# Kernel tuning notes

Measured on AMD Instinct MI355X. Metric: run time of the kernel, lower is better.

Reference implementation:

```python
import jax, jax.numpy as jnp
import numpy as np

NUM_HEADS = 16
SLICE_SIZE = 1024
SCALING = SLICE_SIZE ** 0.5  # module divides by sqrt(slice_size), as written


def setup_inputs() -> dict:
    key = jax.random.key(0)
    ks = jax.random.split(key, 9)
    B, S, D = 4, 2048, SLICE_SIZE
    sc = 0.02
    return {
        "x": jax.random.normal(ks[0], (B, S, D), dtype=jnp.float32),
        "Wq": jax.random.normal(ks[1], (D, D), dtype=jnp.float32) * sc,
        "bq": jax.random.normal(ks[2], (D,), dtype=jnp.float32) * sc,
        "Wk": jax.random.normal(ks[3], (D, D), dtype=jnp.float32) * sc,
        "bk": jax.random.normal(ks[4], (D,), dtype=jnp.float32) * sc,
        "Wv": jax.random.normal(ks[5], (D, D), dtype=jnp.float32) * sc,
        "bv": jax.random.normal(ks[6], (D,), dtype=jnp.float32) * sc,
        "Wp": jax.random.normal(ks[7], (D, D), dtype=jnp.float32) * sc,
        "bp": jax.random.normal(ks[8], (D,), dtype=jnp.float32) * sc,
    }


def _split_heads(t):
    # 'b s (h o) -> b h s o'
    b, s, d = t.shape
    return t.reshape(b, s, NUM_HEADS, d // NUM_HEADS).transpose(0, 2, 1, 3)


def reference(x, Wq, bq, Wk, bk, Wv, bv, Wp, bp):
    q = _split_heads(x @ Wq.T + bq)  # [B,H,S,O]
    k = _split_heads(x @ Wk.T + bk)
    v = _split_heads(x @ Wv.T + bv)
    energy = jnp.einsum('bhqo,bhko->bhqk', q, k)  # full score matrix
    attn = jax.nn.softmax(energy / SCALING, axis=-1)
    # Faithful to source: 'b h q k, b h v o -> b h v o' sums attn over (q,k)
    out = jnp.einsum('bhqk,bhvo->bhvo', attn, v)
    b, h, s, o = out.shape
    out = out.transpose(0, 2, 1, 3).reshape(b, s, h * o)  # 'b h v o -> b v (h o)'
    return out @ Wp.T + bp
```

## Files before the change

kernel.cpp:

```cpp
#include <hip/hip_runtime.h>
#include <cstdint>


typedef unsigned short u16;
typedef __bf16 bf16x8 __attribute__((ext_vector_type(8)));
typedef float f32x4 __attribute__((ext_vector_type(4)));

__device__ __forceinline__ u16 f2bf(float f) {
  unsigned int u = __float_as_uint(f);
  u += 0x7fffu + ((u >> 16) & 1u);
  return (u16)(u >> 16);
}

__device__ __forceinline__ void load16(const void* g, void* l) {
  auto gp = (const __attribute__((address_space(1))) unsigned int*)(uintptr_t)g;
  auto lp = (__attribute__((address_space(3))) unsigned int*)(unsigned int)(uintptr_t)l;
  __builtin_amdgcn_global_load_lds(gp, lp, 16, 0, 0);
}

__global__ void k_prep(const float* __restrict__ x, const float* __restrict__ Wv,
                       const float* __restrict__ bv, const float* __restrict__ Wp,
                       const float* __restrict__ bp, u16* __restrict__ xb,
                       u16* __restrict__ wpb, u16* __restrict__ wvtb,
                       float* __restrict__ cv) {
  __shared__ float tile[32][33];
  const int b = blockIdx.x;
  const int tid = threadIdx.x;
  if (b < 9216) {
    const float* src = (b < 8192) ? x : Wp;
    u16* dst = (b < 8192) ? xb : wpb;
    const long base = (long)((b < 8192) ? b : (b - 8192)) * 1024 + tid * 4;
    const float4 v = *(const float4*)(src + base);
    ushort4 o;
    o.x = f2bf(v.x); o.y = f2bf(v.y); o.z = f2bf(v.z); o.w = f2bf(v.w);
    *(ushort4*)(dst + base) = o;
  } else if (b < 10240) {
    const int tb = b - 9216;
    const int bi = (tb & 31) * 32;
    const int bj = (tb >> 5) * 32;
    const int tx = tid & 31;
    const int ty = tid >> 5;
    for (int r = ty; r < 32; r += 8)
      tile[r][tx] = Wv[(long)(bj + r) * 1024 + bi + tx];
    __syncthreads();
    for (int r = ty; r < 32; r += 8)
      wvtb[(long)(bi + r) * 1024 + bj + tx] = f2bf(tile[tx][r]);
  } else {
    const int row = (b - 10240) * 4 + (tid >> 6);
    const int lane = tid & 63;
    const float* w = Wp + (long)row * 1024;
    float s = 0.f;
    for (int j = lane; j < 1024; j += 64) s += w[j] * bv[j];
    for (int off = 32; off; off >>= 1) s += __shfl_down(s, off, 64);
    if (lane == 0) cv[row] = 2048.f * s + bp[row];
  }
}

template <int MODE>
__global__ __launch_bounds__(256) void k_gemm(
    const u16* __restrict__ A, const u16* __restrict__ B, void* __restrict__ OutV,
    const float* __restrict__ bias, int M, int N, int K) {
  __shared__ u16 As[2][128 * 64];
  __shared__ u16 Bs[2][128 * 64];

  const int tid = threadIdx.x;
  const int lane = tid & 63;
  const int wv = tid >> 6;
  const int waveM = (wv & 1) << 6;
  const int waveN = (wv >> 1) << 6;
  const int l15 = lane & 15;
  const int quad = lane >> 4;

  long bm, bn;
  if constexpr (MODE == 0) {
    const int id = blockIdx.x;
    const int xcd = id & 7;
    const int j = id >> 3;
    const int nb = N >> 7;
    const int mPerXcd = M / 128 / 8;
    bm = (long)(xcd * mPerXcd + j / nb) * 128;
    bn = (long)(j % nb) * 128;
  } else {
    bm = (long)(blockIdx.x >> 3) * 128;
    bn = (long)(blockIdx.x & 7) * 128;
  }

  const int rsl = lane >> 3;
  const int cs = (lane & 7) ^ rsl;
  const u16* Ag0 = A + (bm + wv * 8 + rsl) * (long)K + cs * 8;
  const u16* Bg0 = B + (bn + wv * 8 + rsl) * (long)K + cs * 8;

  const int nT = K >> 6;

  auto STAGE = [&](long k0, int b) {
    u16* Ad = &As[b][0] + (wv << 9);
    u16* Bd = &Bs[b][0] + (wv << 9);
#pragma unroll
    for (int r = 0; r < 4; ++r) {
      load16(Ag0 + k0 + (long)(r * 32) * K, Ad + (r << 11));
      load16(Bg0 + k0 + (long)(r * 32) * K, Bd + (r << 11));
    }
  };

  const f32x4 zero = {0.f, 0.f, 0.f, 0.f};
  f32x4 acc[4][4];
#pragma unroll
  for (int i = 0; i < 4; ++i)
#pragma unroll
    for (int j = 0; j < 4; ++j) acc[i][j] = zero;

  const int rq0 = quad ^ (l15 & 7);
  const int rq1 = (4 + quad) ^ (l15 & 7);

  STAGE(0, 0);
  asm volatile("s_waitcnt vmcnt(0)" ::: "memory");
  __builtin_amdgcn_s_barrier();

  int cur = 0;
  for (int t = 0; t < nT; ++t) {
    const bool more = (t + 1) < nT;
    if (more) STAGE((long)(t + 1) << 6, cur ^ 1);
    __builtin_amdgcn_sched_barrier(0);

    const u16* Asb = &As[cur][0];
    const u16* Bsb = &Bs[cur][0];
    bf16x8 af[2][4], bg[2][4];
#pragma unroll
    for (int tt = 0; tt < 4; ++tt) {
      const int ra = (waveM + tt * 16 + l15) * 64;
      const int rb = (waveN + tt * 16 + l15) * 64;
      af[0][tt] = *(const bf16x8*)(Asb + ra + rq0 * 8);
      af[1][tt] = *(const bf16x8*)(Asb + ra + rq1 * 8);
      bg[0][tt] = *(const bf16x8*)(Bsb + rb + rq0 * 8);
      bg[1][tt] = *(const bf16x8*)(Bsb + rb + rq1 * 8);
    }
    asm volatile("s_waitcnt lgkmcnt(0)" ::: "memory");
    __builtin_amdgcn_sched_barrier(0);

#pragma unroll
    for (int kk = 0; kk < 2; ++kk)
#pragma unroll
      for (int i = 0; i < 4; ++i)
#pragma unroll
        for (int j = 0; j < 4; ++j)
          acc[i][j] = __builtin_amdgcn_mfma_f32_16x16x32_bf16(af[kk][i], bg[kk][j],
                                                              acc[i][j], 0, 0, 0);

    if (more) {
      asm volatile("s_waitcnt vmcnt(0)" ::: "memory");
      __builtin_amdgcn_s_barrier();
      cur ^= 1;
    }
  }

#pragma unroll
  for (int i = 0; i < 4; ++i) {
    const long gm = bm + waveM + i * 16 + quad * 4;
#pragma unroll
    for (int j = 0; j < 4; ++j) {
      const long gn = bn + waveN + j * 16 + l15;
      if constexpr (MODE == 0) {
        float* outp = (float*)OutV;
        const float bb = bias[gn];
#pragma unroll
        for (int r = 0; r < 4; ++r)
          outp[(gm + r) * N + gn] = acc[i][j][r] + bb;
      } else {
        u16* outp = (u16*)OutV;
#pragma unroll
        for (int r = 0; r < 4; ++r)
          outp[(gm + r) * N + gn] = f2bf(acc[i][j][r] * 2048.f);
      }
    }
  }
}

extern "C" void kernel_launch(void* const* d_in, const int* in_sizes, int n_in,
                              void* d_out, int out_size, void* d_ws, size_t ws_size,
                              hipStream_t stream) {
  const float* x  = (const float*)d_in[0];
  const float* Wv = (const float*)d_in[5];
  const float* bv = (const float*)d_in[6];
  const float* Wp = (const float*)d_in[7];
  const float* bp = (const float*)d_in[8];

  char* ws = (char*)d_ws;
  u16* xb    = (u16*)(ws);
  u16* wpb   = (u16*)(ws + (16u << 20));
  u16* wvtb  = (u16*)(ws + (18u << 20));
  u16* m2b   = (u16*)(ws + (20u << 20));
  float* cv  = (float*)(ws + (22u << 20));

  k_prep<<<10496, 256, 0, stream>>>(x, Wv, bv, Wp, bp, xb, wpb, wvtb, cv);

  k_gemm<1><<<64, 256, 0, stream>>>(wpb, wvtb, m2b, nullptr, 1024, 1024, 1024);

  k_gemm<0><<<512, 256, 0, stream>>>(xb, m2b, d_out, cv, 8192, 1024, 1024);
}
```

Baseline: 140.5 us.

## Deepen GEMM pipeline to four-stage LDS ring with K=32 tiles

Changes the GEMM mainloop from a double-buffered K=64 tile to a four-buffer ring of K=32 tiles with three tiles prefetched in flight. Partial vmcnt waits let global loads overlap more iterations of MFMA work, aimed at hiding memory latency in the load-bound GEMMs. The swizzle pattern is reworked for the narrower rows. Each iteration now has half the MFMA work per barrier, which doubles the number of barriers and may reduce LDS read efficiency.

New measurement: 144.8 us. +3.0%, slower.

```diff
diff --git a/kernel.cpp b/kernel.cpp
--- a/kernel.cpp
+++ b/kernel.cpp
@@ -60,8 +60,8 @@
 __global__ __launch_bounds__(256) void k_gemm(
     const u16* __restrict__ A, const u16* __restrict__ B, void* __restrict__ OutV,
     const float* __restrict__ bias, int M, int N, int K) {
-  __shared__ u16 As[2][128 * 64];
-  __shared__ u16 Bs[2][128 * 64];
+  __shared__ u16 As[4][128 * 32];
+  __shared__ u16 Bs[4][128 * 32];
 
   const int tid = threadIdx.x;
   const int lane = tid & 63;
@@ -85,21 +85,22 @@
     bn = (long)(blockIdx.x & 7) * 128;
   }
 
-  const int rsl = lane >> 3;
-  const int cs = (lane & 7) ^ rsl;
-  const u16* Ag0 = A + (bm + wv * 8 + rsl) * (long)K + cs * 8;
-  const u16* Bg0 = B + (bn + wv * 8 + rsl) * (long)K + cs * 8;
+  const int rl = lane >> 2;
+  const int cs = (lane & 3) ^ ((lane >> 3) & 3);
+  const u16* Ag0 = A + (bm + wv * 16 + rl) * (long)K + cs * 8;
+  const u16* Bg0 = B + (bn + wv * 16 + rl) * (long)K + cs * 8;
+  const long rowOff = 64 * (long)K;
 
-  const int nT = K >> 6;
+  const int nT = K >> 5;
 
-  auto STAGE = [&](long k0, int b) {
-    u16* Ad = &As[b][0] + (wv << 9);
-    u16* Bd = &Bs[b][0] + (wv << 9);
-#pragma unroll
-    for (int r = 0; r < 4; ++r) {
-      load16(Ag0 + k0 + (long)(r * 32) * K, Ad + (r << 11));
-      load16(Bg0 + k0 + (long)(r * 32) * K, Bd + (r << 11));
-    }
+  auto STAGE = [&](int tt) {
+    const long k0 = (long)tt << 5;
+    u16* Ad = &As[tt & 3][0] + (wv << 9);
+    u16* Bd = &Bs[tt & 3][0] + (wv << 9);
+    load16(Ag0 + k0, Ad);
+    load16(Ag0 + rowOff + k0, Ad + 2048);
+    load16(Bg0 + k0, Bd);
+    load16(Bg0 + rowOff + k0, Bd + 2048);
   };
 
   const f32x4 zero = {0.f, 0.f, 0.f, 0.f};
@@ -109,47 +110,40 @@
 #pragma unroll
     for (int j = 0; j < 4; ++j) acc[i][j] = zero;
 
-  const int rq0 = quad ^ (l15 & 7);
-  const int rq1 = (4 + quad) ^ (l15 & 7);
+  const int rq = quad ^ ((l15 >> 1) & 3);
 
-  STAGE(0, 0);
-  asm volatile("s_waitcnt vmcnt(0)" ::: "memory");
+  STAGE(0); STAGE(1); STAGE(2);
+  asm volatile("s_waitcnt vmcnt(8)" ::: "memory");
   __builtin_amdgcn_s_barrier();
 
-  int cur = 0;
   for (int t = 0; t < nT; ++t) {
-    const bool more = (t + 1) < nT;
-    if (more) STAGE((long)(t + 1) << 6, cur ^ 1);
+    const int rem = nT - 1 - t;
+    if (rem >= 3) STAGE(t + 3);
     __builtin_amdgcn_sched_barrier(0);
 
-    const u16* Asb = &As[cur][0];
-    const u16* Bsb = &Bs[cur][0];
-    bf16x8 af[2][4], bg[2][4];
+    const u16* Asb = &As[t & 3][0];
+    const u16* Bsb = &Bs[t & 3][0];
+    bf16x8 af[4], bg[4];
 #pragma unroll
-    for (int tt = 0; tt < 4; ++tt) {
-      const int ra = (waveM + tt * 16 + l15) * 64;
-      const int rb = (waveN + tt * 16 + l15) * 64;
-      af[0][tt] = *(const bf16x8*)(Asb + ra + rq0 * 8);
-      af[1][tt] = *(const bf16x8*)(Asb + ra + rq1 * 8);
-      bg[0][tt] = *(const bf16x8*)(Bsb + rb + rq0 * 8);
-      bg[1][tt] = *(const bf16x8*)(Bsb + rb + rq1 * 8);
+    for (int q = 0; q < 4; ++q) {
+      af[q] = *(const bf16x8*)(Asb + (waveM + q * 16 + l15) * 32 + rq * 8);
+      bg[q] = *(const bf16x8*)(Bsb + (waveN + q * 16 + l15) * 32 + rq * 8);
     }
     asm volatile("s_waitcnt lgkmcnt(0)" ::: "memory");
     __builtin_amdgcn_sched_barrier(0);
 
 #pragma unroll
-    for (int kk = 0; kk < 2; ++kk)
+    for (int i = 0; i < 4; ++i)
 #pragma unroll
-      for (int i = 0; i < 4; ++i)
-#pragma unroll
-        for (int j = 0; j < 4; ++j)
-          acc[i][j] = __builtin_amdgcn_mfma_f32_16x16x32_bf16(af[kk][i], bg[kk][j],
-                                                              acc[i][j], 0, 0, 0);
+      for (int j = 0; j < 4; ++j)
+        acc[i][j] = __builtin_amdgcn_mfma_f32_16x16x32_bf16(af[i], bg[j],
+                                                            acc[i][j], 0, 0, 0);
 
-    if (more) {
-      asm volatile("s_waitcnt vmcnt(0)" ::: "memory");
+    if (rem > 0) {
+      if (rem >= 3)      asm volatile("s_waitcnt vmcnt(8)" ::: "memory");
+      else if (rem == 2) asm volatile("s_waitcnt vmcnt(4)" ::: "memory");
+      else               asm volatile("s_waitcnt vmcnt(0)" ::: "memory");
       __builtin_amdgcn_s_barrier();
-      cur ^= 1;
     }
   }
 
```

## Retile GEMMs: 64x64 tiles for weight fold, 8-wave blocks for main GEMM

Applied to the files above, without the earlier changes.

The small weight-folding GEMM now uses 64x64 tiles with 256 blocks instead of 64 blocks of 128x128, so more CUs get work. The main GEMM keeps 128x128 tiles but uses 512 threads (8 waves, each 64x32), which halves per-wave accumulator registers and raises waves per CU. Staging is rewritten so each thread loads contiguous rows with an XOR swizzle. The trade-off is less MFMA work per wave to hide LDS latency, plus more barrier participants per block.

Result: no change. 137.7 us, median of 2 (-2.0%).

```diff
diff --git a/kernel.cpp b/kernel.cpp
--- a/kernel.cpp
+++ b/kernel.cpp
@@ -57,17 +57,26 @@
 }
 
 template <int MODE>
-__global__ __launch_bounds__(256) void k_gemm(
+__global__ __launch_bounds__(MODE == 0 ? 512 : 256) void k_gemm(
     const u16* __restrict__ A, const u16* __restrict__ B, void* __restrict__ OutV,
     const float* __restrict__ bias, int M, int N, int K) {
-  __shared__ u16 As[2][128 * 64];
-  __shared__ u16 Bs[2][128 * 64];
+  constexpr int BM = (MODE == 0) ? 128 : 64;
+  constexpr int BN = (MODE == 0) ? 128 : 64;
+  constexpr int T  = (MODE == 0) ? 512 : 256;
+  constexpr int WTM = (MODE == 0) ? 64 : 32;
+  constexpr int WTN = 32;
+  constexpr int AccM = WTM / 16;
+  constexpr int AccN = WTN / 16;
+  constexpr int RPC = T / 8;
+
+  __shared__ u16 As[2][BM * 64];
+  __shared__ u16 Bs[2][BN * 64];
 
   const int tid = threadIdx.x;
   const int lane = tid & 63;
   const int wv = tid >> 6;
-  const int waveM = (wv & 1) << 6;
-  const int waveN = (wv >> 1) << 6;
+  const int waveM = (wv & 1) * WTM;
+  const int waveN = (wv >> 1) * WTN;
   const int l15 = lane & 15;
   const int quad = lane >> 4;
 
@@ -81,33 +90,32 @@
     bm = (long)(xcd * mPerXcd + j / nb) * 128;
     bn = (long)(j % nb) * 128;
   } else {
-    bm = (long)(blockIdx.x >> 3) * 128;
-    bn = (long)(blockIdx.x & 7) * 128;
-  }
-
-  const int rsl = lane >> 3;
-  const int cs = (lane & 7) ^ rsl;
-  const u16* Ag0 = A + (bm + wv * 8 + rsl) * (long)K + cs * 8;
-  const u16* Bg0 = B + (bn + wv * 8 + rsl) * (long)K + cs * 8;
+    bm = (long)(blockIdx.x >> 4) * 64;
+    bn = (long)(blockIdx.x & 15) * 64;
+  }
+
+  const int rl = tid >> 3;
+  const int cs = (tid & 7) ^ (rl & 7);
+  const u16* Ag0 = A + (bm + rl) * (long)K + cs * 8;
+  const u16* Bg0 = B + (bn + rl) * (long)K + cs * 8;
 
   const int nT = K >> 6;
 
   auto STAGE = [&](long k0, int b) {
-    u16* Ad = &As[b][0] + (wv << 9);
-    u16* Bd = &Bs[b][0] + (wv << 9);
-#pragma unroll
-    for (int r = 0; r < 4; ++r) {
-      load16(Ag0 + k0 + (long)(r * 32) * K, Ad + (r << 11));
-      load16(Bg0 + k0 + (long)(r * 32) * K, Bd + (r << 11));
-    }
+    u16* Ad = &As[b][0] + tid * 8;
+    u16* Bd = &Bs[b][0] + tid * 8;
+    load16(Ag0 + k0, Ad);
+    load16(Ag0 + k0 + (long)RPC * K, Ad + RPC * 64);
+    load16(Bg0 + k0, Bd);
+    load16(Bg0 + k0 + (long)RPC * K, Bd + RPC * 64);
   };
 
   const f32x4 zero = {0.f, 0.f, 0.f, 0.f};
-  f32x4 acc[4][4];
-#pragma unroll
-  for (int i = 0; i < 4; ++i)
-#pragma unroll
-    for (int j = 0; j < 4; ++j) acc[i][j] = zero;
+  f32x4 acc[AccM][AccN];
+#pragma unroll
+  for (int i = 0; i < AccM; ++i)
+#pragma unroll
+    for (int j = 0; j < AccN; ++j) acc[i][j] = zero;
 
   const int rq0 = quad ^ (l15 & 7);
   const int rq1 = (4 + quad) ^ (l15 & 7);
@@ -124,15 +132,18 @@
 
     const u16* Asb = &As[cur][0];
     const u16* Bsb = &Bs[cur][0];
-    bf16x8 af[2][4], bg[2][4];
-#pragma unroll
-    for (int tt = 0; tt < 4; ++tt) {
-      const int ra = (waveM + tt * 16 + l15) * 64;
-      const int rb = (waveN + tt * 16 + l15) * 64;
-      af[0][tt] = *(const bf16x8*)(Asb + ra + rq0 * 8);
-      af[1][tt] = *(const bf16x8*)(Asb + ra + rq1 * 8);
-      bg[0][tt] = *(const bf16x8*)(Bsb + rb + rq0 * 8);
-      bg[1][tt] = *(const bf16x8*)(Bsb + rb + rq1 * 8);
+    bf16x8 af[2][AccM], bg[2][AccN];
+#pragma unroll
+    for (int i = 0; i < AccM; ++i) {
+      const int ra = (waveM + i * 16 + l15) * 64;
+      af[0][i] = *(const bf16x8*)(Asb + ra + rq0 * 8);
+      af[1][i] = *(const bf16x8*)(Asb + ra + rq1 * 8);
+    }
+#pragma unroll
+    for (int j = 0; j < AccN; ++j) {
+      const int rb = (waveN + j * 16 + l15) * 64;
+      bg[0][j] = *(const bf16x8*)(Bsb + rb + rq0 * 8);
+      bg[1][j] = *(const bf16x8*)(Bsb + rb + rq1 * 8);
     }
     asm volatile("s_waitcnt lgkmcnt(0)" ::: "memory");
     __builtin_amdgcn_sched_barrier(0);
@@ -140,9 +151,9 @@
 #pragma unroll
     for (int kk = 0; kk < 2; ++kk)
 #pragma unroll
-      for (int i = 0; i < 4; ++i)
-#pragma unroll
-        for (int j = 0; j < 4; ++j)
+      for (int i = 0; i < AccM; ++i)
+#pragma unroll
+        for (int j = 0; j < AccN; ++j)
           acc[i][j] = __builtin_amdgcn_mfma_f32_16x16x32_bf16(af[kk][i], bg[kk][j],
                                                               acc[i][j], 0, 0, 0);
 
@@ -154,10 +165,10 @@
   }
 
 #pragma unroll
-  for (int i = 0; i < 4; ++i) {
+  for (int i = 0; i < AccM; ++i) {
     const long gm = bm + waveM + i * 16 + quad * 4;
 #pragma unroll
-    for (int j = 0; j < 4; ++j) {
+    for (int j = 0; j < AccN; ++j) {
       const long gn = bn + waveN + j * 16 + l15;
       if constexpr (MODE == 0) {
         float* outp = (float*)OutV;
@@ -193,7 +204,7 @@
 
   k_prep<<<10496, 256, 0, stream>>>(x, Wv, bv, Wp, bp, xb, wpb, wvtb, cv);
 
-  k_gemm<1><<<64, 256, 0, stream>>>(wpb, wvtb, m2b, nullptr, 1024, 1024, 1024);
-
-  k_gemm<0><<<512, 256, 0, stream>>>(xb, m2b, d_out, cv, 8192, 1024, 1024);
-}
+  k_gemm<1><<<256, 256, 0, stream>>>(wpb, wvtb, m2b, nullptr, 1024, 1024, 1024);
+
+  k_gemm<0><<<512, 512, 0, stream>>>(xb, m2b, d_out, cv, 8192, 1024, 1024);
+}
```
